# Kernel optimization log

Hardware: AMD Instinct MI355X
Metric: run time of the kernel (lower is better)

The kernel has to match this reference:

```python
import jax, jax.numpy as jnp
import numpy as np
import math

B, T, J, D2 = 32, 512, 43, 2
DM, H, FF, E, NC = 512, 8, 2048, 101, 100  # d_model, heads, ffn, n_experts(=max_output_len+1), classes


def _ln(x, g, b, eps=1e-5):
    mu = x.mean(-1, keepdims=True)
    var = ((x - mu) ** 2).mean(-1, keepdims=True)
    return (x - mu) / jnp.sqrt(var + eps) * g + b


def _pos_encoding(t, d):
    pos = jnp.arange(t, dtype=jnp.float32)[:, None]
    div = jnp.exp(jnp.arange(0, d, 2, dtype=jnp.float32) * (-math.log(10000.0) / d))
    pe = jnp.zeros((t, d), dtype=jnp.float32)
    pe = pe.at[:, 0::2].set(jnp.sin(pos * div))
    pe = pe.at[:, 1::2].set(jnp.cos(pos * div))
    return pe


def _mha(x, qkv_w, qkv_b, ow, ob, heads):
    b_, t_, d_ = x.shape
    dh = d_ // heads
    qkv = x @ qkv_w.T + qkv_b
    q, k, v = jnp.split(qkv, 3, axis=-1)
    sh = lambda a: a.reshape(b_, t_, heads, dh).transpose(0, 2, 1, 3)
    q, k, v = sh(q), sh(k), sh(v)
    s = jnp.einsum('bhqd,bhkd->bhqk', q, k) / jnp.sqrt(jnp.asarray(dh, x.dtype))
    a = jax.nn.softmax(s, axis=-1)
    ctx = jnp.einsum('bhqk,bhkd->bhqd', a, v).transpose(0, 2, 1, 3).reshape(b_, t_, d_)
    return ctx @ ow.T + ob


def _conv1d(x, w, b):  # x: [B,C,T], w: [O,I,3]
    y = jax.lax.conv_general_dilated(x, w, (1,), [(1, 1)], dimension_numbers=('NCH', 'OIH', 'NCH'))
    return y + b[None, :, None]


def _avgpool2(x):  # [B,C,T] -> [B,C,T//2]
    b_, c_, t_ = x.shape
    return x.reshape(b_, c_, t_ // 2, 2).mean(-1)


def _expert(pos, qkv_w, qkv_b, ow, ob, ng, nb, lw, lb, memory):
    m = memory + pos  # pos: [D], broadcast over [B,Tp,D]
    out = _mha(m, qkv_w, qkv_b, ow, ob, heads=1)
    c = out.mean(axis=1)           # [B,D]
    c = _ln(c, ng, nb)
    return c @ lw.T + lb           # [B,D]


_experts_vmapped = jax.vmap(_expert, in_axes=(0,) * 9 + (None,))


def _forward(poses, W_in, b_in,
             eq_w, eq_b, eo_w, eo_b, ef1_w, ef1_b, ef2_w, ef2_b,
             en1_g, en1_b, en2_g, en2_b,
             c1_w, c1_b, c2_w, c2_b, mlp_w, mlp_b,
             xp_pos, xp_qkv_w, xp_qkv_b, xp_o_w, xp_o_b, xp_n_g, xp_n_b, xp_l_w, xp_l_b,
             fn_g, fn_b, hd_w, hd_b):
    b_, t_, j_, d2_ = poses.shape
    x = poses.reshape(b_, t_, j_ * d2_)
    x = x @ W_in.T + b_in                          # [B,T,DM]
    x = x + _pos_encoding(t_, DM)[None]
    # 2-layer post-norm transformer encoder (torch default: relu FFN, norm after residual)
    for i in range(2):
        a = _mha(x, eq_w[i], eq_b[i], eo_w[i], eo_b[i], heads=H)
        x = _ln(x + a, en1_g[i], en1_b[i])
        ff = jax.nn.relu(x @ ef1_w[i].T + ef1_b[i]) @ ef2_w[i].T + ef2_b[i]
        x = _ln(x + ff, en2_g[i], en2_b[i])
    # temporal pooling: conv-gelu-pool x2  -> [B,DM,T/4]
    y = x.transpose(0, 2, 1)
    y = _avgpool2(jax.nn.gelu(_conv1d(y, c1_w, c1_b), approximate=False))
    y = _avgpool2(jax.nn.gelu(_conv1d(y, c2_w, c2_b), approximate=False))
    mem = y.transpose(0, 2, 1)                      # [B,T/4,DM]
    mem = jax.nn.gelu(mem @ mlp_w.T + mlp_b, approximate=False)
    # all position experts in one batched call: [E,B,DM]
    ctx = _experts_vmapped(xp_pos, xp_qkv_w, xp_qkv_b, xp_o_w, xp_o_b,
                           xp_n_g, xp_n_b, xp_l_w, xp_l_b, mem)
    ctx = _ln(ctx, fn_g, fn_b)
    logits = ctx @ hd_w.T + hd_b                    # [E,B,NC]
    return logits.transpose(1, 0, 2)                # [B,E,NC]


def setup_inputs() -> dict:
    key = jax.random.key(0)
    ks = iter(jax.random.split(key, 64))
    nrm = lambda shape, s=0.02: jax.random.normal(next(ks), shape, dtype=jnp.float32) * s
    inp = {
        'poses': jax.random.normal(next(ks), (B, T, J, D2), dtype=jnp.float32),
        'W_in': nrm((DM, J * D2)), 'b_in': jnp.zeros((DM,)),
        'eq_w': nrm((2, 3 * DM, DM)), 'eq_b': jnp.zeros((2, 3 * DM)),
        'eo_w': nrm((2, DM, DM)), 'eo_b': jnp.zeros((2, DM)),
        'ef1_w': nrm((2, FF, DM)), 'ef1_b': jnp.zeros((2, FF)),
        'ef2_w': nrm((2, DM, FF)), 'ef2_b': jnp.zeros((2, DM)),
        'en1_g': jnp.ones((2, DM)), 'en1_b': jnp.zeros((2, DM)),
        'en2_g': jnp.ones((2, DM)), 'en2_b': jnp.zeros((2, DM)),
        'c1_w': nrm((DM, DM, 3)), 'c1_b': jnp.zeros((DM,)),
        'c2_w': nrm((DM, DM, 3)), 'c2_b': jnp.zeros((DM,)),
        'mlp_w': nrm((DM, DM)), 'mlp_b': jnp.zeros((DM,)),
        'xp_pos': nrm((E, DM)),
        'xp_qkv_w': nrm((E, 3 * DM, DM)), 'xp_qkv_b': jnp.zeros((E, 3 * DM)),
        'xp_o_w': nrm((E, DM, DM)), 'xp_o_b': jnp.zeros((E, DM)),
        'xp_n_g': jnp.ones((E, DM)), 'xp_n_b': jnp.zeros((E, DM)),
        'xp_l_w': nrm((E, DM, DM)), 'xp_l_b': jnp.zeros((E, DM)),
        'fn_g': jnp.ones((DM,)), 'fn_b': jnp.zeros((DM,)),
        'hd_w': nrm((NC, DM)), 'hd_b': jnp.zeros((NC,)),
    }
    return inp


def reference(poses, W_in, b_in,
              eq_w, eq_b, eo_w, eo_b, ef1_w, ef1_b, ef2_w, ef2_b,
              en1_g, en1_b, en2_g, en2_b,
              c1_w, c1_b, c2_w, c2_b, mlp_w, mlp_b,
              xp_pos, xp_qkv_w, xp_qkv_b, xp_o_w, xp_o_b, xp_n_g, xp_n_b, xp_l_w, xp_l_b,
              fn_g, fn_b, hd_w, hd_b):
    return _forward(poses, W_in, b_in,
                    eq_w, eq_b, eo_w, eo_b, ef1_w, ef1_b, ef2_w, ef2_b,
                    en1_g, en1_b, en2_g, en2_b,
                    c1_w, c1_b, c2_w, c2_b, mlp_w, mlp_b,
                    xp_pos, xp_qkv_w, xp_qkv_b, xp_o_w, xp_o_b, xp_n_g, xp_n_b, xp_l_w, xp_l_b,
                    fn_g, fn_b, hd_w, hd_b)
```

## Files before the change

### kernel.cpp

```cpp
#include <hip/hip_runtime.h>
#include <math.h>

typedef unsigned short u16;
typedef __bf16 bf16_t;
typedef bf16_t bf16x8 __attribute__((ext_vector_type(8)));
typedef float f32x4v __attribute__((ext_vector_type(4)));
typedef u16 u16x8 __attribute__((ext_vector_type(8)));
typedef u16 u16x4 __attribute__((ext_vector_type(4)));

__device__ inline u16 f2bf(float f){ __bf16 h=(__bf16)f; return __builtin_bit_cast(u16,h); }
__device__ inline float bf2f(u16 u){ unsigned int x=((unsigned int)u)<<16; return __builtin_bit_cast(float,x); }

#define GLD16(gp,lp) __builtin_amdgcn_global_load_lds( \
  (const __attribute__((address_space(1))) void*)(gp), \
  (__attribute__((address_space(3))) void*)(lp), 16, 0, 0)

#define MFMA_B16(a,b,c) __builtin_amdgcn_mfma_f32_16x16x32_bf16(a,b,c,0,0,0)

struct GP {
  const u16* A; int lda; long long sA1, sA2;
  const u16* B; int ldb; long long sB1, sB2;
  const float* bias; long long sb1, sb2, sbg;
  float* Cf; u16* Cb; int ldc; long long sC1, sC2;
  int M, N, K, Z2, epi, perm;
  float alpha;
};

__device__ inline float epiF(float v,int epi){
  if(epi==1) return fmaxf(v,0.f);
  if(epi==2) return 0.5f*v*(1.f+erff(v*0.70710678118654752f));
  return v;
}

__global__ __launch_bounds__(256) void gemm_bt(GP p){
  __shared__ u16 L[3*8192];
  const int z=blockIdx.z, z1=z/p.Z2, z2=z-z1*p.Z2;
  const u16* __restrict__ Ab = p.A + z1*p.sA1 + z2*p.sA2;
  const u16* __restrict__ Bb = p.B + z1*p.sB1 + z2*p.sB2;
  const int tm=blockIdx.x*128, tn=blockIdx.y*128;
  const int t=threadIdx.x, lane=t&63, wv=t>>6;
  const int wr=(wv>>1)*64, wc=(wv&1)*64;
  const int fr=lane&15, c16=lane>>4;

  long long aoff[2], boff[2];
  #pragma unroll
  for(int q=0;q<2;q++){
    int s=(wv*2+q)*64+lane;
    int r=s>>2;
    int col=((s&3)^((r>>1)&3))*8;
    int ga=tm+r; if(ga>p.M-1) ga=p.M-1;
    int gb=tn+r; if(gb>p.N-1) gb=p.N-1;
    aoff[q]=(long long)ga*p.lda+col;
    boff[q]=(long long)gb*p.ldb+col;
  }

  auto STAGE=[&](int tk,int buf){
    const long long kk=(long long)tk*32;
    u16* base=&L[buf*8192];
    #pragma unroll
    for(int q=0;q<2;q++){
      GLD16(Ab+aoff[q]+kk, base+(wv*2+q)*512);
      GLD16(Bb+boff[q]+kk, base+4096+(wv*2+q)*512);
    }
  };

  const int nt = p.K >> 5;
  f32x4v acc[4][4]={};

  STAGE(0,0);
  if(nt>1){
    STAGE(1,1);
    asm volatile("s_waitcnt vmcnt(4)" ::: "memory");
  } else {
    asm volatile("s_waitcnt vmcnt(0)" ::: "memory");
  }
  __builtin_amdgcn_s_barrier();
  __builtin_amdgcn_sched_barrier(0);

  for(int i=0;i<nt;++i){
    const int buf=i%3;
    if(i+2<nt) STAGE(i+2,(i+2)%3);
    const u16* Abuf=&L[buf*8192];
    const u16* Bbuf=&L[buf*8192+4096];
    bf16x8 af[4], bfv[4];
    #pragma unroll
    for(int m=0;m<4;m++){ int r=wr+16*m+fr; af[m]=*(const bf16x8*)&Abuf[r*32+((c16^((r>>1)&3))*8)]; }
    #pragma unroll
    for(int n=0;n<4;n++){ int r=wc+16*n+fr; bfv[n]=*(const bf16x8*)&Bbuf[r*32+((c16^((r>>1)&3))*8)]; }
    #pragma unroll
    for(int m=0;m<4;m++)
      #pragma unroll
      for(int n=0;n<4;n++)
        acc[m][n]=MFMA_B16(af[m],bfv[n],acc[m][n]);
    if(i+1<nt){
      if(i+2<nt) asm volatile("s_waitcnt vmcnt(4)" ::: "memory");
      else       asm volatile("s_waitcnt vmcnt(0)" ::: "memory");
      __builtin_amdgcn_s_barrier();
      __builtin_amdgcn_sched_barrier(0);
    }
  }

  const int rq=lane>>4;
  const long long cbase = z1*p.sC1 + z2*p.sC2;
  float* __restrict__ Cf = p.Cf? p.Cf+cbase : nullptr;
  u16*  __restrict__ Cbp = p.Cb? p.Cb+cbase : nullptr;

  const bool vec = (!p.perm) && (p.epi!=3) && ((p.N&63)==0) && !(Cf&&Cbp);
  if(vec){
    float bvn[4];
    #pragma unroll
    for(int n=0;n<4;n++){
      int gc=tn+wc+n*16+fr; if(gc>p.N-1) gc=p.N-1;
      bvn[n]=p.bias? p.bias[z1*p.sb1+z2*p.sb2+(long long)gc*p.sbg] : 0.f;
    }
    if(Cbp){
      u16* my=(u16*)L + wv*1024;
      #pragma unroll
      for(int m=0;m<4;m++){
        __syncthreads();
        #pragma unroll
        for(int n=0;n<4;n++){
          int pg=((n^rq)<<4)+fr;
          #pragma unroll
          for(int r=0;r<4;r++)
            my[(4*rq+r)*64+pg]=f2bf(epiF(acc[m][n][r]*p.alpha+bvn[n],p.epi));
        }
        __syncthreads();
        #pragma unroll
        for(int ps=0;ps<2;ps++){
          int row=ps*8+(lane>>3), h=lane&7;
          int grow=tm+wr+m*16+row, gc0=tn+wc+h*8;
          if(grow<p.M && gc0<p.N){
            int phys=(((h>>1)^(row>>2))<<4)+((h&1)<<3);
            *(u16x8*)&Cbp[(long long)grow*p.ldc+gc0]=*(const u16x8*)&my[row*64+phys];
          }
        }
      }
    } else {
      float* my=(float*)L + wv*1024;
      #pragma unroll
      for(int m=0;m<4;m++){
        __syncthreads();
        #pragma unroll
        for(int n=0;n<4;n++){
          int pg=((n^rq)<<4)+fr;
          #pragma unroll
          for(int r=0;r<4;r++)
            my[(4*rq+r)*64+pg]=epiF(acc[m][n][r]*p.alpha+bvn[n],p.epi);
        }
        __syncthreads();
        #pragma unroll
        for(int ps=0;ps<2;ps++){
          int row=ps*8+(lane>>3), h=lane&7;
          int grow=tm+wr+m*16+row, gc0=tn+wc+h*8;
          if(grow<p.M && gc0<p.N){
            int phys=(((h>>1)^(row>>2))<<4)+((h&1)<<3);
            *(float4*)&Cf[(long long)grow*p.ldc+gc0]  =*(const float4*)&my[row*64+phys];
            *(float4*)&Cf[(long long)grow*p.ldc+gc0+4]=*(const float4*)&my[row*64+phys+4];
          }
        }
      }
    }
    return;
  }

  #pragma unroll
  for(int m=0;m<4;m++){
    int grow0=tm+wr+16*m+4*rq;
    #pragma unroll
    for(int n=0;n<4;n++){
      int gcol=tn+wc+16*n+fr;
      if(gcol>=p.N) continue;
      float bv = p.bias? p.bias[z1*p.sb1+z2*p.sb2+(long long)gcol*p.sbg] : 0.f;
      #pragma unroll
      for(int r=0;r<4;r++){
        int grow=grow0+r;
        if(grow>=p.M) continue;
        float v=acc[m][n][r]*p.alpha+bv;
        if(p.epi==1) v=fmaxf(v,0.f);
        else if(p.epi==2) v=0.5f*v*(1.f+erff(v*0.70710678118654752f));
        else if(p.epi==3){
          int tt=grow&511;
          float ang=(float)tt*expf((float)(gcol&~1)*(-0.017988946039015967f));
          v += (gcol&1)? cosf(ang) : sinf(ang);
        }
        long long ci;
        if(p.perm) ci = ((long long)((grow&31)*101 + (grow>>5)))*100 + gcol;
        else       ci = (long long)grow*p.ldc+gcol;
        if(Cf) Cf[ci]=v;
        if(Cbp) Cbp[ci]=f2bf(v);
      }
    }
  }
}

__global__ __launch_bounds__(512) void gemm_big8(GP p){
  __shared__ u16 L[65536];
  const int z=blockIdx.z, z1=z/p.Z2, z2=z-z1*p.Z2;
  const u16* __restrict__ Ab = p.A + z1*p.sA1 + z2*p.sA2;
  const u16* __restrict__ Bb = p.B + z1*p.sB1 + z2*p.sB2;
  const int tm=blockIdx.x*256, tn=blockIdx.y*256;
  const int t=threadIdx.x, lane=t&63, wv=t>>6;
  const int wr2=(wv>>2)*128, wc2=(wv&3)*64;
  const int fr=lane&15, c16=lane>>4;

  long long aoff[2], boff[2];
  {
    int rr=t>>2, cs=((t&3)^((t>>3)&3))*8;
    #pragma unroll
    for(int q=0;q<2;q++){
      int ga=tm+q*128+rr; if(ga>p.M-1) ga=p.M-1;
      int gb=tn+q*128+rr; if(gb>p.N-1) gb=p.N-1;
      aoff[q]=(long long)ga*p.lda+cs;
      boff[q]=(long long)gb*p.ldb+cs;
    }
  }

  auto STAGE_A=[&](int kt,int d,int ks){
    const long long k0=(long long)kt*64+ks*32;
    u16* dst=&L[d*16384+ks*8192];
    GLD16(Ab+aoff[0]+k0, dst+t*8);
    GLD16(Ab+aoff[1]+k0, dst+4096+t*8);
  };
  auto STAGE_B=[&](int kt,int d,int ks){
    const long long k0=(long long)kt*64+ks*32;
    u16* dst=&L[32768+d*16384+ks*8192];
    GLD16(Bb+boff[0]+k0, dst+t*8);
    GLD16(Bb+boff[1]+k0, dst+4096+t*8);
  };
  auto LDA_=[&](int d,int ks,int m)->bf16x8{
    int R=wr2+m*16+fr;
    return *(const bf16x8*)&L[d*16384+ks*8192+R*32+((c16^((R>>1)&3))*8)];
  };
  auto LDB_=[&](int d,int ks,int n)->bf16x8{
    int R=wc2+n*16+fr;
    return *(const bf16x8*)&L[32768+d*16384+ks*8192+R*32+((c16^((R>>1)&3))*8)];
  };

  const int ntk=p.K>>6;
  f32x4v acc[8][4]={};
  bf16x8 af[8], bq0, bq1, bq2, bq3;

  STAGE_A(0,0,0); STAGE_B(0,0,0); STAGE_A(0,0,1); STAGE_B(0,0,1);
  asm volatile("s_waitcnt vmcnt(4)" ::: "memory");
  __builtin_amdgcn_s_barrier();
  __builtin_amdgcn_sched_barrier(0);

  for(int kt=0;kt<ntk;++kt){
    const int d=kt&1, nd=d^1;
    const bool nxt=(kt+1<ntk);
    #pragma unroll
    for(int m=0;m<8;m++) af[m]=LDA_(d,0,m);
    bq0=LDB_(d,0,0); bq1=LDB_(d,0,1);
    if(nxt) STAGE_A(kt+1,nd,0);
    __builtin_amdgcn_s_barrier();
    asm volatile("s_waitcnt lgkmcnt(0)" ::: "memory");
    __builtin_amdgcn_sched_barrier(0);
    __builtin_amdgcn_s_setprio(1);
    #pragma unroll
    for(int m=0;m<8;m++){
      acc[m][0]=MFMA_B16(af[m],bq0,acc[m][0]);
      acc[m][1]=MFMA_B16(af[m],bq1,acc[m][1]);
    }
    __builtin_amdgcn_s_setprio(0);
    __builtin_amdgcn_s_barrier();
    bq2=LDB_(d,0,2); bq3=LDB_(d,0,3);
    if(nxt) STAGE_B(kt+1,nd,0);
    __builtin_amdgcn_s_barrier();
    asm volatile("s_waitcnt lgkmcnt(0)" ::: "memory");
    __builtin_amdgcn_sched_barrier(0);
    __builtin_amdgcn_s_setprio(1);
    #pragma unroll
    for(int m=0;m<8;m++){
      acc[m][2]=MFMA_B16(af[m],bq2,acc[m][2]);
      acc[m][3]=MFMA_B16(af[m],bq3,acc[m][3]);
    }
    __builtin_amdgcn_s_setprio(0);
    if(nxt) asm volatile("s_waitcnt vmcnt(4)" ::: "memory");
    else    asm volatile("s_waitcnt vmcnt(0)" ::: "memory");
    __builtin_amdgcn_s_barrier();
    __builtin_amdgcn_sched_barrier(0);
    #pragma unroll
    for(int m=0;m<8;m++) af[m]=LDA_(d,1,m);
    bq0=LDB_(d,1,0); bq1=LDB_(d,1,1);
    if(nxt) STAGE_A(kt+1,nd,1);
    __builtin_amdgcn_s_barrier();
    asm volatile("s_waitcnt lgkmcnt(0)" ::: "memory");
    __builtin_amdgcn_sched_barrier(0);
    __builtin_amdgcn_s_setprio(1);
    #pragma unroll
    for(int m=0;m<8;m++){
      acc[m][0]=MFMA_B16(af[m],bq0,acc[m][0]);
      acc[m][1]=MFMA_B16(af[m],bq1,acc[m][1]);
    }
    __builtin_amdgcn_s_setprio(0);
    __builtin_amdgcn_s_barrier();
    bq2=LDB_(d,1,2); bq3=LDB_(d,1,3);
    if(nxt) STAGE_B(kt+1,nd,1);
    __builtin_amdgcn_s_barrier();
    asm volatile("s_waitcnt lgkmcnt(0)" ::: "memory");
    __builtin_amdgcn_sched_barrier(0);
    __builtin_amdgcn_s_setprio(1);
    #pragma unroll
    for(int m=0;m<8;m++){
      acc[m][2]=MFMA_B16(af[m],bq2,acc[m][2]);
      acc[m][3]=MFMA_B16(af[m],bq3,acc[m][3]);
    }
    __builtin_amdgcn_s_setprio(0);
    if(nxt) asm volatile("s_waitcnt vmcnt(4)" ::: "memory");
    __builtin_amdgcn_s_barrier();
    __builtin_amdgcn_sched_barrier(0);
  }

  const int rq=lane>>4;
  const long long cbase = z1*p.sC1 + z2*p.sC2;
  float* __restrict__ Cf = p.Cf? p.Cf+cbase : nullptr;
  u16*  __restrict__ Cbp = p.Cb? p.Cb+cbase : nullptr;

  const bool vec = (!p.perm) && (p.epi!=3) && ((p.N&63)==0) && !(Cf&&Cbp);
  if(vec){
    float bvn[4];
    #pragma unroll
    for(int n=0;n<4;n++){
      int gc=tn+wc2+n*16+fr; if(gc>p.N-1) gc=p.N-1;
      bvn[n]=p.bias? p.bias[z1*p.sb1+z2*p.sb2+(long long)gc*p.sbg] : 0.f;
    }
    if(Cbp){
      u16* my=(u16*)L + wv*1024;
      #pragma unroll
      for(int m=0;m<8;m++){
        __syncthreads();
        #pragma unroll
        for(int n=0;n<4;n++){
          int pg=((n^rq)<<4)+fr;
          #pragma unroll
          for(int r=0;r<4;r++)
            my[(4*rq+r)*64+pg]=f2bf(epiF(acc[m][n][r]*p.alpha+bvn[n],p.epi));
        }
        __syncthreads();
        #pragma unroll
        for(int ps=0;ps<2;ps++){
          int row=ps*8+(lane>>3), h=lane&7;
          int grow=tm+wr2+m*16+row, gc0=tn+wc2+h*8;
          if(grow<p.M && gc0<p.N){
            int phys=(((h>>1)^(row>>2))<<4)+((h&1)<<3);
            *(u16x8*)&Cbp[(long long)grow*p.ldc+gc0]=*(const u16x8*)&my[row*64+phys];
          }
        }
      }
    } else {
      float* my=(float*)L + wv*1024;
      #pragma unroll
      for(int m=0;m<8;m++){
        __syncthreads();
        #pragma unroll
        for(int n=0;n<4;n++){
          int pg=((n^rq)<<4)+fr;
          #pragma unroll
          for(int r=0;r<4;r++)
            my[(4*rq+r)*64+pg]=epiF(acc[m][n][r]*p.alpha+bvn[n],p.epi);
        }
        __syncthreads();
        #pragma unroll
        for(int ps=0;ps<2;ps++){
          int row=ps*8+(lane>>3), h=lane&7;
          int grow=tm+wr2+m*16+row, gc0=tn+wc2+h*8;
          if(grow<p.M && gc0<p.N){
            int phys=(((h>>1)^(row>>2))<<4)+((h&1)<<3);
            *(float4*)&Cf[(long long)grow*p.ldc+gc0]  =*(const float4*)&my[row*64+phys];
            *(float4*)&Cf[(long long)grow*p.ldc+gc0+4]=*(const float4*)&my[row*64+phys+4];
          }
        }
      }
    }
    return;
  }

  #pragma unroll
  for(int m=0;m<8;m++){
    int grow0=tm+wr2+m*16+4*rq;
    #pragma unroll
    for(int n=0;n<4;n++){
      int gcol=tn+wc2+n*16+fr;
      if(gcol>=p.N) continue;
      float bv = p.bias? p.bias[z1*p.sb1+z2*p.sb2+gcol] : 0.f;
      #pragma unroll
      for(int r=0;r<4;r++){
        int grow=grow0+r;
        if(grow>=p.M) continue;
        float v=epiF(acc[m][n][r]*p.alpha+bv,p.epi);
        long long ci=(long long)grow*p.ldc+gcol;
        if(Cf) Cf[ci]=v;
        if(Cbp) Cbp[ci]=f2bf(v);
      }
    }
  }
}

__global__ __launch_bounds__(256) void softmax512b(u16* __restrict__ S, int nrows){
  int row=blockIdx.x*4+(threadIdx.x>>6);
  if(row>=nrows) return;
  int lane=threadIdx.x&63;
  u16* p=S+(long long)row*512;
  u16x8 raw=*(u16x8*)&p[lane*8];
  float f[8];
  #pragma unroll
  for(int j=0;j<8;j++) f[j]=bf2f(raw[j]);
  float m=f[0];
  #pragma unroll
  for(int j=1;j<8;j++) m=fmaxf(m,f[j]);
  #pragma unroll
  for(int off=32;off;off>>=1) m=fmaxf(m,__shfl_xor(m,off));
  float s=0.f;
  #pragma unroll
  for(int j=0;j<8;j++){ f[j]=__expf(f[j]-m); s+=f[j]; }
  #pragma unroll
  for(int off=32;off;off>>=1) s+=__shfl_xor(s,off);
  float inv=1.f/s;
  u16x8 o;
  #pragma unroll
  for(int j=0;j<8;j++) o[j]=f2bf(f[j]*inv);
  *(u16x8*)&p[lane*8]=o;
}

__global__ __launch_bounds__(256) void ln512(
    const float* __restrict__ x, const float* __restrict__ res,
    const float* __restrict__ g, const float* __restrict__ bb, int pergroup,
    float* __restrict__ outf, u16* __restrict__ outb, int nrows)
{
  int row=blockIdx.x*4+(threadIdx.x>>6);
  if(row>=nrows) return;
  int lane=threadIdx.x&63;
  const float4* xp=(const float4*)(x+(long long)row*512);
  float4 v0=xp[lane], v1=xp[lane+64];
  if(res){
    const float4* rp=(const float4*)(res+(long long)row*512);
    float4 w0=rp[lane], w1=rp[lane+64];
    v0.x+=w0.x; v0.y+=w0.y; v0.z+=w0.z; v0.w+=w0.w;
    v1.x+=w1.x; v1.y+=w1.y; v1.z+=w1.z; v1.w+=w1.w;
  }
  float s=v0.x+v0.y+v0.z+v0.w+v1.x+v1.y+v1.z+v1.w;
  #pragma unroll
  for(int off=32;off;off>>=1) s+=__shfl_xor(s,off);
  float mu=s*(1.f/512.f);
  float q=(v0.x-mu)*(v0.x-mu)+(v0.y-mu)*(v0.y-mu)+(v0.z-mu)*(v0.z-mu)+(v0.w-mu)*(v0.w-mu)
        +(v1.x-mu)*(v1.x-mu)+(v1.y-mu)*(v1.y-mu)+(v1.z-mu)*(v1.z-mu)+(v1.w-mu)*(v1.w-mu);
  #pragma unroll
  for(int off=32;off;off>>=1) q+=__shfl_xor(q,off);
  float rstd=rsqrtf(q*(1.f/512.f)+1e-5f);
  long long go = pergroup? (long long)(row>>5)*512 : 0;
  float4 g0=((const float4*)(g+go))[lane],  g1=((const float4*)(g+go))[lane+64];
  float4 b0=((const float4*)(bb+go))[lane], b1=((const float4*)(bb+go))[lane+64];
  float4 o0,o1;
  o0.x=(v0.x-mu)*rstd*g0.x+b0.x; o0.y=(v0.y-mu)*rstd*g0.y+b0.y;
  o0.z=(v0.z-mu)*rstd*g0.z+b0.z; o0.w=(v0.w-mu)*rstd*g0.w+b0.w;
  o1.x=(v1.x-mu)*rstd*g1.x+b1.x; o1.y=(v1.y-mu)*rstd*g1.y+b1.y;
  o1.z=(v1.z-mu)*rstd*g1.z+b1.z; o1.w=(v1.w-mu)*rstd*g1.w+b1.w;
  if(outf){
    ((float4*)(outf+(long long)row*512))[lane]=o0;
    ((float4*)(outf+(long long)row*512))[lane+64]=o1;
  }
  if(outb){
    u16x4 h0,h1;
    h0[0]=f2bf(o0.x); h0[1]=f2bf(o0.y); h0[2]=f2bf(o0.z); h0[3]=f2bf(o0.w);
    h1[0]=f2bf(o1.x); h1[1]=f2bf(o1.y); h1[2]=f2bf(o1.z); h1[3]=f2bf(o1.w);
    ((u16x4*)(outb+(long long)row*512))[lane]=h0;
    ((u16x4*)(outb+(long long)row*512))[lane+64]=h1;
  }
}

__global__ __launch_bounds__(256) void vtransb(const u16* __restrict__ qkv,
                                               u16* __restrict__ Vt){
  __shared__ u16 tile[64][72];
  int tt=blockIdx.x, h=blockIdx.y, zb=blockIdx.z;
  int t=threadIdx.x;
  int i=t>>2, j0=(t&3)*16;
  const u16* src = qkv + ((long long)(zb*512 + tt*64 + i))*1536 + 1024 + h*64 + j0;
  *(u16x8*)&tile[i][j0]   = *(const u16x8*)&src[0];
  *(u16x8*)&tile[i][j0+8] = *(const u16x8*)&src[8];
  __syncthreads();
  int j=t>>2, i0=(t&3)*16;
  u16 tmp[16];
  #pragma unroll
  for(int c=0;c<16;c++) tmp[c]=tile[i0+c][j];
  u16* dst = Vt + ((long long)((zb*8+h)*64 + j))*512 + tt*64 + i0;
  *(u16x8*)&dst[0]=*(u16x8*)&tmp[0];
  *(u16x8*)&dst[8]=*(u16x8*)&tmp[8];
}

__global__ __launch_bounds__(256) void trcvtb(const float* __restrict__ src,
                                              u16* __restrict__ dst){
  __shared__ float tile[64][65];
  int bi=blockIdx.x, bj=blockIdx.y, z=blockIdx.z;
  int e=z>>1, half=z&1;
  const float* s = src + (long long)e*786432 + half*262144;
  int t=threadIdx.x;
  int i=t>>2, j0=(t&3)*16;
  const float* sp = s + (long long)(bi*64+i)*512 + bj*64 + j0;
  #pragma unroll
  for(int c=0;c<4;c++){
    float4 v=((const float4*)sp)[c];
    tile[i][j0+4*c+0]=v.x; tile[i][j0+4*c+1]=v.y;
    tile[i][j0+4*c+2]=v.z; tile[i][j0+4*c+3]=v.w;
  }
  __syncthreads();
  int j=t>>2, i0=(t&3)*16;
  u16* d = dst + (long long)z*262144 + (long long)(bj*64+j)*512 + bi*64 + i0;
  u16x8 o0,o1;
  #pragma unroll
  for(int c=0;c<8;c++){ o0[c]=f2bf(tile[i0+c][j]); o1[c]=f2bf(tile[i0+8+c][j]); }
  *(u16x8*)&d[0]=o0; *(u16x8*)&d[8]=o1;
}

__global__ __launch_bounds__(256) void im2col3b(const u16* __restrict__ in,
                                                u16* __restrict__ out,
                                                int Tlen, long long n8){
  long long idx=(long long)blockIdx.x*256+threadIdx.x;
  if(idx>=n8) return;
  int i8=(int)(idx&63); long long s=idx>>6;
  int dt=(int)(s%3); long long bt=s/3;
  int tt=(int)(bt%Tlen); int b=(int)(bt/Tlen);
  int tsrc=tt+dt-1;
  u16x8 v={0,0,0,0,0,0,0,0};
  if(tsrc>=0 && tsrc<Tlen) v=*(const u16x8*)&in[((long long)(b*Tlen+tsrc))*512 + i8*8];
  *(u16x8*)&out[idx*8]=v;
}

__global__ __launch_bounds__(256) void wrepackb(const float* __restrict__ w,
                                                u16* __restrict__ out){
  int idx=blockIdx.x*256+threadIdx.x;
  if(idx>=512*1536) return;
  int o=idx/1536; int rem=idx-o*1536;
  int dt=rem/512; int i=rem-dt*512;
  out[idx]=f2bf(w[((long long)o*512+i)*3+dt]);
}

__global__ __launch_bounds__(256) void pool2b(const float* __restrict__ in,
                                              u16* __restrict__ out,
                                              int Tlen, long long n4){
  long long idx=(long long)blockIdx.x*256+threadIdx.x;
  if(idx>=n4) return;
  int c=(int)((idx&127)*4); long long s=idx>>7;
  int half=Tlen/2;
  int tp=(int)(s%half); int b=(int)(s/half);
  const float* p=in+((long long)(b*Tlen+2*tp))*512+c;
  float4 a=*(const float4*)p, d=*(const float4*)(p+512);
  u16x4 o;
  o[0]=f2bf(0.5f*(a.x+d.x)); o[1]=f2bf(0.5f*(a.y+d.y));
  o[2]=f2bf(0.5f*(a.z+d.z)); o[3]=f2bf(0.5f*(a.w+d.w));
  *(u16x4*)&out[(s*512)+c]=o;
}

__global__ __launch_bounds__(256) void cvt_bf16(const float* __restrict__ in,
                                                u16* __restrict__ out, long long n8){
  long long i=(long long)blockIdx.x*256+threadIdx.x;
  if(i>=n8) return;
  const float4* p=(const float4*)(in+i*8);
  float4 a=p[0], b=p[1];
  u16x8 o;
  o[0]=f2bf(a.x); o[1]=f2bf(a.y); o[2]=f2bf(a.z); o[3]=f2bf(a.w);
  o[4]=f2bf(b.x); o[5]=f2bf(b.y); o[6]=f2bf(b.z); o[7]=f2bf(b.w);
  *(u16x8*)(out+i*8)=o;
}

__global__ __launch_bounds__(256) void cvt_wv(const float* __restrict__ in,
                                              u16* __restrict__ out, long long n8){
  long long idx=(long long)blockIdx.x*256+threadIdx.x;
  if(idx>=n8) return;
  int e=(int)(idx>>15); long long r8=idx&32767;
  const float* p=in+(long long)e*786432+524288+r8*8;
  float4 a=((const float4*)p)[0], b=((const float4*)p)[1];
  u16x8 o;
  o[0]=f2bf(a.x); o[1]=f2bf(a.y); o[2]=f2bf(a.z); o[3]=f2bf(a.w);
  o[4]=f2bf(b.x); o[5]=f2bf(b.y); o[6]=f2bf(b.z); o[7]=f2bf(b.w);
  *(u16x8*)(out+idx*8)=o;
}

__global__ __launch_bounds__(256) void cvt_pad(const float* __restrict__ in,
                                               u16* __restrict__ out,
                                               int rows, int ks, int kd){
  long long idx=(long long)blockIdx.x*256+threadIdx.x;
  if(idx>=(long long)rows*kd) return;
  int r=(int)(idx/kd), c=(int)(idx-(long long)r*kd);
  out[idx]=(c<ks)? f2bf(in[(long long)r*ks+c]) : (u16)0;
}

__global__ __launch_bounds__(256) void expert_reduce(
    const u16* __restrict__ S, const u16* __restrict__ mem,
    const float* __restrict__ pos, u16* __restrict__ wout)
{
  int b=blockIdx.x, e=blockIdx.y;
  int t=threadIdx.x, lane=t&63, w=t>>6;
  const u16* Sp = S + ((long long)(e*32+b))*16384;
  __shared__ float abw[4][128];
  __shared__ float abf[128];
  float a0=0.f, a1=0.f;
  for(int q=w*32;q<w*32+32;++q){
    unsigned v2=*(const unsigned*)&Sp[q*128+lane*2];
    float x=bf2f((u16)(v2&0xffff)), y=bf2f((u16)(v2>>16));
    float m=fmaxf(x,y);
    #pragma unroll
    for(int off=32;off;off>>=1) m=fmaxf(m,__shfl_xor(m,off));
    float ex=__expf(x-m), ey=__expf(y-m);
    float s=ex+ey;
    #pragma unroll
    for(int off=32;off;off>>=1) s+=__shfl_xor(s,off);
    float inv=1.f/s;
    a0+=ex*inv; a1+=ey*inv;
  }
  abw[w][2*lane]=a0; abw[w][2*lane+1]=a1;
  __syncthreads();
  if(t<128) abf[t]=(abw[0][t]+abw[1][t]+abw[2][t]+abw[3][t])*(1.f/128.f);
  __syncthreads();
  float c0=0.f, c1=0.f;
  const u16* mb = mem + (long long)b*65536;
  for(int k=0;k<128;++k){
    float a=abf[k];
    c0+=a*bf2f(mb[k*512+t]);
    c1+=a*bf2f(mb[k*512+t+256]);
  }
  c0+=pos[(long long)e*512+t]; c1+=pos[(long long)e*512+t+256];
  u16* o=wout+((long long)e*32+b)*512;
  o[t]=f2bf(c0); o[t+256]=f2bf(c1);
}

static inline int ceildiv(int a,int b){return (a+b-1)/b;}

static GP mkGP(const u16* A,int lda,long long sA1,long long sA2,
  const u16* B,int ldb,long long sB1,long long sB2,
  const float* bias,long long sb1,long long sb2,
  float* Cf,u16* Cb,int ldc,long long sC1,long long sC2,
  int M,int N,int K,int Z2,int epi,float alpha,long long sbg,int perm){
  GP p;
  p.A=A; p.lda=lda; p.sA1=sA1; p.sA2=sA2;
  p.B=B; p.ldb=ldb; p.sB1=sB1; p.sB2=sB2;
  p.bias=bias; p.sb1=sb1; p.sb2=sb2; p.sbg=sbg;
  p.Cf=Cf; p.Cb=Cb; p.ldc=ldc; p.sC1=sC1; p.sC2=sC2;
  p.M=M; p.N=N; p.K=K; p.Z2=Z2; p.epi=epi; p.perm=perm; p.alpha=alpha;
  return p;
}

static void gemmB(hipStream_t s,
  const u16* A,int lda,long long sA1,long long sA2,
  const u16* B,int ldb,long long sB1,long long sB2,
  const float* bias,long long sb1,long long sb2,
  float* Cf,u16* Cb,int ldc,long long sC1,long long sC2,
  int M,int N,int K,int Z,int Z2,int epi,float alpha,
  long long sbg=1,int perm=0){
  GP p=mkGP(A,lda,sA1,sA2,B,ldb,sB1,sB2,bias,sb1,sb2,Cf,Cb,ldc,sC1,sC2,M,N,K,Z2,epi,alpha,sbg,perm);
  dim3 g(ceildiv(M,128), ceildiv(N,128), Z);
  gemm_bt<<<g, dim3(256), 0, s>>>(p);
}

static void gemmBig(hipStream_t s,
  const u16* A,int lda,long long sA1,long long sA2,
  const u16* B,int ldb,long long sB1,long long sB2,
  const float* bias,long long sb1,long long sb2,
  float* Cf,u16* Cb,int ldc,long long sC1,long long sC2,
  int M,int N,int K,int Z,int Z2,int epi,float alpha){
  GP p=mkGP(A,lda,sA1,sA2,B,ldb,sB1,sB2,bias,sb1,sb2,Cf,Cb,ldc,sC1,sC2,M,N,K,Z2,epi,alpha,1,0);
  dim3 g(ceildiv(M,256), ceildiv(N,256), Z);
  gemm_big8<<<g, dim3(512), 0, s>>>(p);
}

static inline void cvt(hipStream_t s, const float* in, u16* out, long long n){
  long long n8=n/8;
  cvt_bf16<<<(int)((n8+255)/256),256,0,s>>>(in,out,n8);
}

#define ALPHA_S 0.044194173824159216f

extern "C" void kernel_launch(void* const* d_in, const int* in_sizes, int n_in,
                              void* d_out, int out_size, void* d_ws, size_t ws_size,
                              hipStream_t stream) {
  (void)in_sizes; (void)n_in; (void)out_size;
  const float* poses=(const float*)d_in[0];
  const float* W_in =(const float*)d_in[1];
  const float* b_in =(const float*)d_in[2];
  const float* eq_w =(const float*)d_in[3];
  const float* eq_b =(const float*)d_in[4];
  const float* eo_w =(const float*)d_in[5];
  const float* eo_b =(const float*)d_in[6];
  const float* ef1_w=(const float*)d_in[7];
  const float* ef1_b=(const float*)d_in[8];
  const float* ef2_w=(const float*)d_in[9];
  const float* ef2_b=(const float*)d_in[10];
  const float* en1_g=(const float*)d_in[11];
  const float* en1_b=(const float*)d_in[12];
  const float* en2_g=(const float*)d_in[13];
  const float* en2_b=(const float*)d_in[14];
  const float* c1_w =(const float*)d_in[15];
  const float* c1_b =(const float*)d_in[16];
  const float* c2_w =(const float*)d_in[17];
  const float* c2_b =(const float*)d_in[18];
  const float* mlp_w=(const float*)d_in[19];
  const float* mlp_b=(const float*)d_in[20];
  const float* xp_pos  =(const float*)d_in[21];
  const float* xp_qkv_w=(const float*)d_in[22];
  const float* xp_qkv_b=(const float*)d_in[23];
  const float* xp_o_w  =(const float*)d_in[24];
  const float* xp_o_b  =(const float*)d_in[25];
  const float* xp_n_g  =(const float*)d_in[26];
  const float* xp_n_b  =(const float*)d_in[27];
  const float* xp_l_w  =(const float*)d_in[28];
  const float* xp_l_b  =(const float*)d_in[29];
  const float* fn_g =(const float*)d_in[30];
  const float* fn_b =(const float*)d_in[31];
  const float* hd_w =(const float*)d_in[32];
  const float* hd_b =(const float*)d_in[33];
  float* out=(float*)d_out;

  float* ws=(float*)d_ws;
  size_t off=0;
  auto alloc=[&](size_t n)->float*{ float* p=ws+off; off+=(n+255)&~(size_t)255; return p; };
  float* RA = alloc(137760768);
  float* RB = alloc(84381184);
  float* RC = alloc(5849088);
  if(off*sizeof(float) > ws_size) return;

  u16* qkvb =(u16*)RA;
  u16* Sb16 =(u16*)(RA+12582912);
  u16* ffb  =(u16*)(RA+46137344);
  u16* ctxb =(u16*)(RA+62914560);
  u16* Vtb  =(u16*)(RA+67108864);
  float* act0f=RA+71303168;
  float* act1f=RA+79691776;
  float* tmpf =RA+88080384;
  u16* act0b=(u16*)(RA+96468992);
  u16* act1b=(u16*)(RA+98566144);
  u16* Pb   =(u16*)RA;
  u16* Sb2  =(u16*)(RA+105906176);
  float* U  =RA+132382720;
  float* ctx1=RA+132796416;
  float* ctx2=RA+134451200;
  u16* ln1b =(u16*)(RA+136105984);
  u16* ln2b =(u16*)(RA+136933376);
  u16* posesb=(u16*)RB;
  u16* W_inb =(u16*)(RB+786432);
  u16* eqwb  =(u16*)(RB+811008);
  u16* eowb  =(u16*)(RB+1597440);
  u16* ef1wb =(u16*)(RB+1859584);
  u16* ef2wb =(u16*)(RB+2908160);
  u16* wc1b  =(u16*)(RB+3956736);
  u16* wc2b  =(u16*)(RB+4349952);
  u16* mlpwb =(u16*)(RB+4743168);
  u16* hdwb  =(u16*)(RB+4874240);
  u16* xposb =(u16*)(RB+4899840);
  u16* owb   =(u16*)(RB+4925696);
  u16* lwb   =(u16*)(RB+18163968);
  u16* wvb   =(u16*)(RB+31402240);
  u16* wqkT  =(u16*)(RB+44640512);
  u16* Gpb   =(u16*)(RB+71117056);
  u16* Hb    =(u16*)(RB+84355328);
  u16* gmemb =(u16*)RC;
  u16* p1b   =(u16*)(RC+1048576);
  u16* membb =(u16*)(RC+3145728);
  u16* wb    =(u16*)(RC+4194304);
  u16* cmeanb=(u16*)(RC+5021696);

  cvt_pad<<<ceildiv(16384*96,256),256,0,stream>>>(poses,posesb,16384,86,96);
  cvt_pad<<<ceildiv(512*96,256),256,0,stream>>>(W_in,W_inb,512,86,96);
  cvt(stream,eq_w,eqwb,1572864);
  cvt(stream,eo_w,eowb,524288);
  cvt(stream,ef1_w,ef1wb,2097152);
  cvt(stream,ef2_w,ef2wb,2097152);
  cvt(stream,mlp_w,mlpwb,262144);
  cvt(stream,hd_w,hdwb,51200);
  cvt(stream,xp_pos,xposb,51712);
  cvt(stream,xp_o_w,owb,26476544);
  cvt(stream,xp_l_w,lwb,26476544);
  wrepackb<<<ceildiv(512*1536,256),256,0,stream>>>(c1_w,wc1b);
  wrepackb<<<ceildiv(512*1536,256),256,0,stream>>>(c2_w,wc2b);
  trcvtb<<<dim3(8,8,202),256,0,stream>>>(xp_qkv_w,wqkT);
  cvt_wv<<<ceildiv(101*32768,256),256,0,stream>>>(xp_qkv_w,wvb,(long long)101*32768);

  gemmB(stream, posesb,96,0,0, W_inb,96,0,0, b_in,0,0,
        act0f,act0b,512,0,0, 16384,512,96, 1,1, 3,1.f);

  for(int l=0;l<2;++l){
    gemmBig(stream, act0b,512,0,0, eqwb+(long long)l*786432,512,0,0,
          eq_b+(long long)l*1536,0,0, nullptr,qkvb,1536,0,0, 16384,1536,512, 1,1, 0,1.f);
    gemmB(stream, qkvb,1536,786432,64, qkvb+512,1536,786432,64, nullptr,0,0,
          nullptr,Sb16,512,2097152,262144, 512,512,64, 256,8, 0,0.125f);
    softmax512b<<<32768,256,0,stream>>>(Sb16,131072);
    vtransb<<<dim3(8,8,32),256,0,stream>>>(qkvb,Vtb);
    gemmB(stream, Sb16,512,2097152,262144, Vtb,512,262144,32768, nullptr,0,0,
          nullptr,ctxb,512,262144,64, 512,64,512, 256,8, 0,1.f);
    gemmBig(stream, ctxb,512,0,0, eowb+(long long)l*262144,512,0,0,
          eo_b+(long long)l*512,0,0, tmpf,nullptr,512,0,0, 16384,512,512, 1,1, 0,1.f);
    ln512<<<4096,256,0,stream>>>(tmpf,act0f,en1_g+(long long)l*512,en1_b+(long long)l*512,0,
                                 act1f,act1b,16384);
    gemmBig(stream, act1b,512,0,0, ef1wb+(long long)l*1048576,512,0,0,
          ef1_b+(long long)l*2048,0,0, nullptr,ffb,2048,0,0, 16384,2048,512, 1,1, 1,1.f);
    gemmBig(stream, ffb,2048,0,0, ef2wb+(long long)l*1048576,2048,0,0,
          ef2_b+(long long)l*512,0,0, tmpf,nullptr,512,0,0, 16384,512,2048, 1,1, 0,1.f);
    ln512<<<4096,256,0,stream>>>(tmpf,act1f,en2_g+(long long)l*512,en2_b+(long long)l*512,0,
                                 act0f,act0b,16384);
  }

  u16* Ccb=(u16*)RA;
  im2col3b<<<(int)(((long long)16384*1536/8+255)/256),256,0,stream>>>(act0b,Ccb,512,(long long)16384*1536/8);
  gemmBig(stream, Ccb,1536,0,0, wc1b,1536,0,0, c1_b,0,0,
        tmpf,nullptr,512,0,0, 16384,512,1536, 1,1, 2,1.f);
  pool2b<<<(int)(((long long)32*256*128+255)/256),256,0,stream>>>(tmpf,p1b,512,(long long)32*256*128);
  im2col3b<<<(int)(((long long)8192*1536/8+255)/256),256,0,stream>>>(p1b,Ccb,256,(long long)8192*1536/8);
  gemmBig(stream, Ccb,1536,0,0, wc2b,1536,0,0, c2_b,0,0,
        tmpf,nullptr,512,0,0, 8192,512,1536, 1,1, 2,1.f);
  pool2b<<<(int)(((long long)32*128*128+255)/256),256,0,stream>>>(tmpf,membb,256,(long long)32*128*128);
  gemmBig(stream, membb,512,0,0, mlpwb,512,0,0, mlp_b,0,0,
        nullptr,gmemb,512,0,0, 4096,512,512, 1,1, 2,1.f);

  gemmBig(stream, wqkT+262144,512,524288,0, wqkT,512,524288,0, nullptr,0,0,
        nullptr,Gpb,512,262144,0, 512,512,512, 101,1, 0,1.f);
  gemmB(stream, Gpb,512,262144,0, xposb,512,512,0, nullptr,0,0,
        nullptr,Hb,1,512,0, 512,1,512, 101,1, 0,1.f);
  gemmB(stream, gmemb,512,0,0, Hb,512,0,0, nullptr,0,0,
        U,nullptr,101,0,0, 4096,101,512, 1,1, 0,ALPHA_S);
  gemmBig(stream, gmemb,512,0,0, Gpb,512,262144,0, nullptr,0,0,
        nullptr,Pb,512,2097152,0, 4096,512,512, 101,1, 0,1.f);
  gemmB(stream, Pb,512,2097152,65536, gmemb,512,0,65536, U,1,12928,
        nullptr,Sb2,128,524288,16384, 128,128,512, 3232,32, 0,ALPHA_S, 101);
  expert_reduce<<<dim3(32,101),256,0,stream>>>(Sb2,gmemb,xp_pos,wb);
  gemmB(stream, wb,512,16384,0, wvb,512,262144,0, xp_qkv_b+1024,1536,0,
        nullptr,cmeanb,512,16384,0, 32,512,512, 101,1, 0,1.f);

  gemmB(stream, cmeanb,512,16384,0, owb,512,262144,0, xp_o_b,512,0,
        ctx1,nullptr,512,16384,0, 32,512,512, 101,1, 0,1.f);
  ln512<<<808,256,0,stream>>>(ctx1,nullptr,xp_n_g,xp_n_b,1, nullptr,ln1b,3232);
  gemmB(stream, ln1b,512,16384,0, lwb,512,262144,0, xp_l_b,512,0,
        ctx2,nullptr,512,16384,0, 32,512,512, 101,1, 0,1.f);
  ln512<<<808,256,0,stream>>>(ctx2,nullptr,fn_g,fn_b,0, nullptr,ln2b,3232);
  gemmB(stream, ln2b,512,0,0, hdwb,512,0,0, hd_b,0,0,
        out,nullptr,100,0,0, 3232,100,512, 1,1, 0,1.f, 1,1);
}
```

Before: 2.101 ms.

## Fuse expert score GEMM with softmax and column-mean reduction

Adds a dedicated 128x128 GEMM kernel that computes per-(expert,batch) attention scores, then applies the row softmax and column mean in shared memory. It writes only a 128-float mean vector per block instead of the full bf16 score matrix. This removes the write and re-read of roughly 3232x128x128 scores and moves the softmax/mean out of expert_reduce. The trade-off is a fixed, less tuned GEMM loop and a large LDS footprint of about 66KB per block, which may limit occupancy. Softmax is also now computed on fp32 scores rather than bf16-rounded ones.

```diff
diff --git a/kernel.cpp b/kernel.cpp
--- a/kernel.cpp
+++ b/kernel.cpp
@@ -16,6 +16,7 @@
   (__attribute__((address_space(3))) void*)(lp), 16, 0, 0)
 
 #define MFMA_B16(a,b,c) __builtin_amdgcn_mfma_f32_16x16x32_bf16(a,b,c,0,0,0)
+#define ALPHA_S 0.044194173824159216f
 
 struct GP {
   const u16* A; int lda; long long sA1, sA2;
@@ -194,6 +195,107 @@
   }
 }
 
+__global__ __launch_bounds__(256) void gemm_sfused(
+    const u16* __restrict__ Pm, const u16* __restrict__ mem,
+    const float* __restrict__ U, float* __restrict__ abar){
+  __shared__ float Sl[128*129];
+  u16* L=(u16*)Sl;
+  const int z=blockIdx.x, e=z>>5, b=z&31;
+  const u16* __restrict__ Ab = Pm + (long long)e*2097152 + (long long)b*65536;
+  const u16* __restrict__ Bb = mem + (long long)b*65536;
+  const int t=threadIdx.x, lane=t&63, wv=t>>6;
+  const int wr=(wv>>1)*64, wc=(wv&1)*64;
+  const int fr=lane&15, c16=lane>>4;
+
+  long long aoff[2], boff[2];
+  #pragma unroll
+  for(int q=0;q<2;q++){
+    int s=(wv*2+q)*64+lane;
+    int r=s>>2;
+    int col=((s&3)^((r>>1)&3))*8;
+    aoff[q]=(long long)r*512+col;
+    boff[q]=(long long)r*512+col;
+  }
+  auto STAGE=[&](int tk,int buf){
+    const long long kk=(long long)tk*32;
+    u16* base=&L[buf*8192];
+    #pragma unroll
+    for(int q=0;q<2;q++){
+      GLD16(Ab+aoff[q]+kk, base+(wv*2+q)*512);
+      GLD16(Bb+boff[q]+kk, base+4096+(wv*2+q)*512);
+    }
+  };
+
+  f32x4v acc[4][4]={};
+  STAGE(0,0);
+  STAGE(1,1);
+  asm volatile("s_waitcnt vmcnt(4)" ::: "memory");
+  __builtin_amdgcn_s_barrier();
+  __builtin_amdgcn_sched_barrier(0);
+
+  for(int i=0;i<16;++i){
+    const int buf=i%3;
+    if(i+2<16) STAGE(i+2,(i+2)%3);
+    const u16* Abuf=&L[buf*8192];
+    const u16* Bbuf=&L[buf*8192+4096];
+    bf16x8 af[4], bfv[4];
+    #pragma unroll
+    for(int m=0;m<4;m++){ int r=wr+16*m+fr; af[m]=*(const bf16x8*)&Abuf[r*32+((c16^((r>>1)&3))*8)]; }
+    #pragma unroll
+    for(int n=0;n<4;n++){ int r=wc+16*n+fr; bfv[n]=*(const bf16x8*)&Bbuf[r*32+((c16^((r>>1)&3))*8)]; }
+    #pragma unroll
+    for(int m=0;m<4;m++)
+      #pragma unroll
+      for(int n=0;n<4;n++)
+        acc[m][n]=MFMA_B16(af[m],bfv[n],acc[m][n]);
+    if(i+1<16){
+      if(i+2<16) asm volatile("s_waitcnt vmcnt(4)" ::: "memory");
+      else       asm volatile("s_waitcnt vmcnt(0)" ::: "memory");
+      __builtin_amdgcn_s_barrier();
+      __builtin_amdgcn_sched_barrier(0);
+    }
+  }
+
+  const int rq=lane>>4;
+  float bvn[4];
+  #pragma unroll
+  for(int n=0;n<4;n++){
+    int col=wc+n*16+fr;
+    bvn[n]=U[((long long)(b*128+col))*101+e];
+  }
+  __syncthreads();
+  #pragma unroll
+  for(int m=0;m<4;m++)
+    #pragma unroll
+    for(int n=0;n<4;n++){
+      int col=wc+n*16+fr;
+      #pragma unroll
+      for(int r=0;r<4;r++){
+        int row=wr+m*16+4*rq+r;
+        Sl[row*129+col]=acc[m][n][r]*ALPHA_S+bvn[n];
+      }
+    }
+  __syncthreads();
+  {
+    int row=t>>1, h=t&1;
+    float* pr=&Sl[row*129+h*64];
+    float mx=pr[0];
+    for(int j=1;j<64;j++) mx=fmaxf(mx,pr[j]);
+    mx=fmaxf(mx,__shfl_xor(mx,1));
+    float s=0.f;
+    for(int j=0;j<64;j++){ float ex=__expf(pr[j]-mx); pr[j]=ex; s+=ex; }
+    s+=__shfl_xor(s,1);
+    float inv=1.f/s;
+    for(int j=0;j<64;j++) pr[j]*=inv;
+  }
+  __syncthreads();
+  if(t<128){
+    float s=0.f;
+    for(int r=0;r<128;r++) s+=Sl[r*129+t];
+    abar[(long long)z*128+t]=s*(1.f/128.f);
+  }
+}
+
 __global__ __launch_bounds__(512) void gemm_big8(GP p){
   __shared__ u16 L[65536];
   const int z=blockIdx.z, z1=z/p.Z2, z2=z-z1*p.Z2;
@@ -585,32 +687,14 @@
   out[idx]=(c<ks)? f2bf(in[(long long)r*ks+c]) : (u16)0;
 }
 
-__global__ __launch_bounds__(256) void expert_reduce(
-    const u16* __restrict__ S, const u16* __restrict__ mem,
+__global__ __launch_bounds__(256) void expert_reduce2(
+    const float* __restrict__ abar, const u16* __restrict__ mem,
     const float* __restrict__ pos, u16* __restrict__ wout)
 {
   int b=blockIdx.x, e=blockIdx.y;
-  int t=threadIdx.x, lane=t&63, w=t>>6;
-  const u16* Sp = S + ((long long)(e*32+b))*16384;
-  __shared__ float abw[4][128];
+  int t=threadIdx.x;
   __shared__ float abf[128];
-  float a0=0.f, a1=0.f;
-  for(int q=w*32;q<w*32+32;++q){
-    unsigned v2=*(const unsigned*)&Sp[q*128+lane*2];
-    float x=bf2f((u16)(v2&0xffff)), y=bf2f((u16)(v2>>16));
-    float m=fmaxf(x,y);
-    #pragma unroll
-    for(int off=32;off;off>>=1) m=fmaxf(m,__shfl_xor(m,off));
-    float ex=__expf(x-m), ey=__expf(y-m);
-    float s=ex+ey;
-    #pragma unroll
-    for(int off=32;off;off>>=1) s+=__shfl_xor(s,off);
-    float inv=1.f/s;
-    a0+=ex*inv; a1+=ey*inv;
-  }
-  abw[w][2*lane]=a0; abw[w][2*lane+1]=a1;
-  __syncthreads();
-  if(t<128) abf[t]=(abw[0][t]+abw[1][t]+abw[2][t]+abw[3][t])*(1.f/128.f);
+  if(t<128) abf[t]=abar[((long long)(e*32+b))*128+t];
   __syncthreads();
   float c0=0.f, c1=0.f;
   const u16* mb = mem + (long long)b*65536;
@@ -667,8 +751,6 @@
   long long n8=n/8;
   cvt_bf16<<<(int)((n8+255)/256),256,0,s>>>(in,out,n8);
 }
-
-#define ALPHA_S 0.044194173824159216f
 
 extern "C" void kernel_launch(void* const* d_in, const int* in_sizes, int n_in,
                               void* d_out, int out_size, void* d_ws, size_t ws_size,
@@ -729,7 +811,7 @@
   u16* act0b=(u16*)(RA+96468992);
   u16* act1b=(u16*)(RA+98566144);
   u16* Pb   =(u16*)RA;
-  u16* Sb2  =(u16*)(RA+105906176);
+  float* abarf=RA+105906176;
   float* U  =RA+132382720;
   float* ctx1=RA+132796416;
   float* ctx2=RA+134451200;
@@ -818,9 +900,8 @@
         U,nullptr,101,0,0, 4096,101,512, 1,1, 0,ALPHA_S);
   gemmBig(stream, gmemb,512,0,0, Gpb,512,262144,0, nullptr,0,0,
         nullptr,Pb,512,2097152,0, 4096,512,512, 101,1, 0,1.f);
-  gemmB(stream, Pb,512,2097152,65536, gmemb,512,0,65536, U,1,12928,
-        nullptr,Sb2,128,524288,16384, 128,128,512, 3232,32, 0,ALPHA_S, 101);
-  expert_reduce<<<dim3(32,101),256,0,stream>>>(Sb2,gmemb,xp_pos,wb);
+  gemm_sfused<<<3232,256,0,stream>>>(Pb, gmemb, U, abarf);
+  expert_reduce2<<<dim3(32,101),256,0,stream>>>(abarf,gmemb,xp_pos,wb);
   gemmB(stream, wb,512,16384,0, wvb,512,262144,0, xp_qkv_b+1024,1536,0,
         nullptr,cmeanb,512,16384,0, 32,512,512, 101,1, 0,1.f);
 
```

After: 2.028 ms (median of 2 runs). -3.5%, faster.
